# Optimization experiments

Measured on AMD Instinct MI355X. Metric: run time of the kernel, lower is better.

Reference implementation:

```python
import jax, jax.numpy as jnp
import numpy as np

INPUT_SIZE = 2048
HIDDEN_SIZE = 2048
BATCH = 4096


def setup_inputs() -> dict:
    key = jax.random.key(0)
    ks = jax.random.split(key, 24)
    s_in = 1.0 / np.sqrt(INPUT_SIZE)
    s_h = 1.0 / np.sqrt(HIDDEN_SIZE)
    inp = {
        "x": jax.random.normal(ks[0], (BATCH, INPUT_SIZE), jnp.float32),
        "h_prev": jax.random.normal(ks[1], (BATCH, HIDDEN_SIZE), jnp.float32),
        "c_prev": jax.random.normal(ks[2], (BATCH, HIDDEN_SIZE), jnp.float32),
        "n_prev": jnp.ones((BATCH, HIDDEN_SIZE), jnp.float32),
        "m_prev": jnp.zeros((BATCH, HIDDEN_SIZE), jnp.float32),
    }
    # 4 input projections (W*x) and 4 recurrent projections (R*h), each Linear w/ bias.
    names_x = ["Wzx", "Wix", "Wfx", "Wox"]
    names_h = ["Rzh", "Rih", "Rfh", "Roh"]
    for j, n in enumerate(names_x):
        inp[n + "_w"] = jax.random.uniform(ks[3 + 2 * j], (HIDDEN_SIZE, INPUT_SIZE), jnp.float32, -s_in, s_in)
        inp[n + "_b"] = jax.random.uniform(ks[4 + 2 * j], (HIDDEN_SIZE,), jnp.float32, -s_in, s_in)
    for j, n in enumerate(names_h):
        inp[n + "_w"] = jax.random.uniform(ks[11 + 2 * j], (HIDDEN_SIZE, HIDDEN_SIZE), jnp.float32, -s_h, s_h)
        inp[n + "_b"] = jax.random.uniform(ks[12 + 2 * j], (HIDDEN_SIZE,), jnp.float32, -s_h, s_h)
    return inp


def _lin(x, w, b):
    return x @ w.T + b


def reference(x, h_prev, c_prev, n_prev, m_prev,
              Wzx_w, Wzx_b, Wix_w, Wix_b, Wfx_w, Wfx_b, Wox_w, Wox_b,
              Rzh_w, Rzh_b, Rih_w, Rih_b, Rfh_w, Rfh_b, Roh_w, Roh_b):
    z = jnp.tanh(_lin(x, Wzx_w, Wzx_b) + _lin(h_prev, Rzh_w, Rzh_b))
    # log(i) and log(f) are the pre-activations (i = exp(pre_i), f = exp(pre_f))
    log_i = _lin(x, Wix_w, Wix_b) + _lin(h_prev, Rih_w, Rih_b)
    log_f = _lin(x, Wfx_w, Wfx_b) + _lin(h_prev, Rfh_w, Rfh_b)
    o = jax.nn.sigmoid(_lin(x, Wox_w, Wox_b) + _lin(h_prev, Roh_w, Roh_b))
    m = jnp.maximum(log_f + m_prev, log_i)  # stabilizer state
    i_hat = jnp.exp(log_i - m)
    f_hat = jnp.exp(log_f + m_prev - m)
    c = f_hat * c_prev + i_hat * z
    n = f_hat * n_prev + i_hat
    h = o * c / n
    return (h, c, n, m)
```

## Files before the change

### kernel.cpp

```cpp
#include <hip/hip_runtime.h>
#include <hip/hip_bf16.h>


#define BATCH 4096
#define NHID  2048
#define KDIM  4096
#define NTOT  8388608L
#define AW_OFS 16777216
#define BUFSZ 24576

typedef float  f32x4   __attribute__((ext_vector_type(4)));
typedef short  short8  __attribute__((ext_vector_type(8)));
typedef unsigned short ushort8 __attribute__((ext_vector_type(8)));

#define GL_LDS16(gp, lp)                                                      \
    __builtin_amdgcn_global_load_lds(                                         \
        (const __attribute__((address_space(1))) void*)(gp),                  \
        (__attribute__((address_space(3))) void*)(lp), 16, 0, 0)

__device__ __forceinline__ unsigned short f2bf(float f) {
    unsigned u = __float_as_uint(f);
    unsigned r = (u + 0x7fffu + ((u >> 16) & 1u)) >> 16;
    return (unsigned short)r;
}

__global__ void convA_kernel(const float* __restrict__ x,
                             const float* __restrict__ h,
                             unsigned short* __restrict__ A) {
    int gid = blockIdx.x * 256 + threadIdx.x;
    int row = gid >> 9;
    int col = (gid & 511) << 3;
    const float* src = (col < 2048) ? (x + (long)row * 2048 + col)
                                    : (h + (long)row * 2048 + (col - 2048));
    f32x4 v0 = __builtin_nontemporal_load((const f32x4*)src);
    f32x4 v1 = __builtin_nontemporal_load((const f32x4*)src + 1);
    ushort8 o;
    o[0] = f2bf(v0[0]); o[1] = f2bf(v0[1]); o[2] = f2bf(v0[2]); o[3] = f2bf(v0[3]);
    o[4] = f2bf(v1[0]); o[5] = f2bf(v1[1]); o[6] = f2bf(v1[2]); o[7] = f2bf(v1[3]);
    *(ushort8*)(A + ((long)row << 12) + col) = o;
}

__global__ void convW_kernel(const float* __restrict__ w0, const float* __restrict__ w1,
                             const float* __restrict__ w2, const float* __restrict__ w3,
                             const float* __restrict__ w4, const float* __restrict__ w5,
                             const float* __restrict__ w6, const float* __restrict__ w7,
                             unsigned short* __restrict__ Wb) {
    int z = blockIdx.y;
    const float* src;
    switch (z) {
        case 0: src = w0; break; case 1: src = w1; break;
        case 2: src = w2; break; case 3: src = w3; break;
        case 4: src = w4; break; case 5: src = w5; break;
        case 6: src = w6; break; default: src = w7; break;
    }
    int gid = blockIdx.x * 256 + threadIdx.x;
    int row = gid >> 8;
    int col = (gid & 255) << 3;
    const float* p = src + (long)row * 2048 + col;
    f32x4 v0 = __builtin_nontemporal_load((const f32x4*)p);
    f32x4 v1 = __builtin_nontemporal_load((const f32x4*)p + 1);
    ushort8 o;
    o[0] = f2bf(v0[0]); o[1] = f2bf(v0[1]); o[2] = f2bf(v0[2]); o[3] = f2bf(v0[3]);
    o[4] = f2bf(v1[0]); o[5] = f2bf(v1[1]); o[6] = f2bf(v1[2]); o[7] = f2bf(v1[3]);
    int g = z & 3, hf = z >> 2;
    *(ushort8*)(Wb + (long)g * NHID * KDIM + (long)row * KDIM + hf * 2048 + col) = o;
}

__global__ void bias_kernel(const float* __restrict__ b0, const float* __restrict__ b1,
                            const float* __restrict__ b2, const float* __restrict__ b3,
                            const float* __restrict__ r0, const float* __restrict__ r1,
                            const float* __restrict__ r2, const float* __restrict__ r3,
                            float* __restrict__ Bb) {
    int gid = blockIdx.x * 256 + threadIdx.x;
    int g = gid >> 11, j = gid & 2047;
    const float *wb, *rb;
    switch (g) {
        case 0: wb = b0; rb = r0; break; case 1: wb = b1; rb = r1; break;
        case 2: wb = b2; rb = r2; break; default: wb = b3; rb = r3; break;
    }
    Bb[gid] = wb[j] + rb[j];
}

__global__ __launch_bounds__(512, 4) void slstm_kernel(
    const __hip_bfloat16* __restrict__ A,
    const float* __restrict__ Bb,
    const float* __restrict__ c_prev,
    const float* __restrict__ n_prev,
    const float* __restrict__ m_prev,
    float* __restrict__ out)
{
    __shared__ uint4 smem4[(2 * BUFSZ) / 16];
    char* smem = (char*)smem4;

    const int tid  = threadIdx.x;
    const int lane = tid & 63;
    const int wv   = tid >> 6;
    const int gate = wv & 3;
    const int rh   = wv >> 2;
    const int lm   = lane & 15;
    const int quad = lane >> 4;

    const int row0 = blockIdx.x * 128;
    const int col0 = blockIdx.y * 64;

    const int cof   = ((quad ^ (lm & 3))) * 16;
    const int abase = (rh * 64 + lm) * 64 + cof;
    const int bbase = 8192 + (gate * 64 + lm) * 64 + cof;

    int gofs[3], lofs[3];
#pragma unroll
    for (int t = 0; t < 3; ++t) {
        int id = wv * 3 + t;
        if (id < 8) {
            int idx = id * 64 + lane;
            int r = idx >> 2, jj = idx & 3;
            int j = jj ^ (r & 3);
            gofs[t] = (row0 + r) * KDIM + j * 8;
            lofs[t] = idx * 16;
        } else {
            int idx = (id - 8) * 64 + lane;
            int gr = idx >> 2, jj = idx & 3;
            int g = gr >> 6, rr = gr & 63;
            int j = jj ^ (gr & 3);
            gofs[t] = AW_OFS + (g * NHID + col0 + rr) * KDIM + j * 8;
            lofs[t] = 8192 + idx * 16;
        }
    }

    f32x4 acc[4][4];
#pragma unroll
    for (int mt = 0; mt < 4; ++mt)
#pragma unroll
        for (int nt = 0; nt < 4; ++nt)
#pragma unroll
            for (int r = 0; r < 4; ++r) acc[mt][nt][r] = 0.0f;

#pragma unroll
    for (int t = 0; t < 3; ++t) {
        GL_LDS16(A + gofs[t], smem + lofs[t]);
        gofs[t] += 32;
    }

    for (int kt = 0; kt < 128; ++kt) {
        asm volatile("s_waitcnt vmcnt(0)" ::: "memory");
        __builtin_amdgcn_s_barrier();

        const char* cur = smem + (kt & 1) * BUFSZ;
        char*       wrt = smem + ((kt & 1) ^ 1) * BUFSZ;

        if (kt < 127) {
#pragma unroll
            for (int t = 0; t < 3; ++t) {
                GL_LDS16(A + gofs[t], wrt + lofs[t]);
                gofs[t] += 32;
            }
        }

        short8 af[4], bf[4];
#pragma unroll
        for (int mt = 0; mt < 4; ++mt)
            af[mt] = *(const short8*)(cur + abase + mt * 1024);
#pragma unroll
        for (int nt = 0; nt < 4; ++nt)
            bf[nt] = *(const short8*)(cur + bbase + nt * 1024);
#pragma unroll
        for (int mt = 0; mt < 4; ++mt)
#pragma unroll
            for (int nt = 0; nt < 4; ++nt)
                acc[mt][nt] = __builtin_amdgcn_mfma_f32_16x16x32_bf16(
                    af[mt], bf[nt], acc[mt][nt], 0, 0, 0);
    }

    float* exch = (float*)smem;
#pragma unroll
    for (int mt = 0; mt < 4; ++mt) {
        __syncthreads();
#pragma unroll
        for (int nt = 0; nt < 4; ++nt)
#pragma unroll
            for (int r = 0; r < 4; ++r)
                exch[((rh * 4 + gate) * 16 + quad * 4 + r) * 65 + nt * 16 + lm] =
                    acc[mt][nt][r];
        __syncthreads();
#pragma unroll
        for (int q = 0; q < 4; ++q) {
            int e   = q * 512 + tid;
            int erh = e >> 10, row = (e >> 6) & 15, col = e & 63;
            int R = row0 + erh * 64 + mt * 16 + row;
            int C = col0 + col;
            long idx = (long)R * NHID + C;
            float zp = exch[((erh * 4 + 0) * 16 + row) * 65 + col] + Bb[C];
            float ip = exch[((erh * 4 + 1) * 16 + row) * 65 + col] + Bb[2048 + C];
            float fp = exch[((erh * 4 + 2) * 16 + row) * 65 + col] + Bb[4096 + C];
            float op = exch[((erh * 4 + 3) * 16 + row) * 65 + col] + Bb[6144 + C];
            float cp = __builtin_nontemporal_load(c_prev + idx);
            float np = __builtin_nontemporal_load(n_prev + idx);
            float mp = __builtin_nontemporal_load(m_prev + idx);
            float z  = tanhf(zp);
            float o  = 1.0f / (1.0f + __expf(-op));
            float mm = fmaxf(fp + mp, ip);
            float ih = __expf(ip - mm);
            float fh = __expf(fp + mp - mm);
            float cc = fh * cp + ih * z;
            float nn = fh * np + ih;
            float hh = o * cc / nn;
            __builtin_nontemporal_store(hh, out + idx);
            __builtin_nontemporal_store(cc, out + NTOT + idx);
            __builtin_nontemporal_store(nn, out + 2 * NTOT + idx);
            __builtin_nontemporal_store(mm, out + 3 * NTOT + idx);
        }
    }
}

extern "C" void kernel_launch(void* const* d_in, const int* in_sizes, int n_in,
                              void* d_out, int out_size, void* d_ws, size_t ws_size,
                              hipStream_t stream) {
    const float* x      = (const float*)d_in[0];
    const float* h_prev = (const float*)d_in[1];
    const float* c_prev = (const float*)d_in[2];
    const float* n_prev = (const float*)d_in[3];
    const float* m_prev = (const float*)d_in[4];
    unsigned short* A  = (unsigned short*)d_ws;
    unsigned short* Wb = (unsigned short*)((char*)d_ws + 33554432);
    float*          Bb = (float*)((char*)d_ws + 100663296);

    convA_kernel<<<8192, 256, 0, stream>>>(x, h_prev, A);
    convW_kernel<<<dim3(2048, 8), 256, 0, stream>>>(
        (const float*)d_in[5], (const float*)d_in[7], (const float*)d_in[9],
        (const float*)d_in[11], (const float*)d_in[13], (const float*)d_in[15],
        (const float*)d_in[17], (const float*)d_in[19], Wb);
    bias_kernel<<<32, 256, 0, stream>>>(
        (const float*)d_in[6], (const float*)d_in[8], (const float*)d_in[10],
        (const float*)d_in[12], (const float*)d_in[14], (const float*)d_in[16],
        (const float*)d_in[18], (const float*)d_in[20], Bb);

    slstm_kernel<<<dim3(32, 32), 512, 0, stream>>>(
        (const __hip_bfloat16*)A, Bb, c_prev, n_prev, m_prev, (float*)d_out);
}
```

Baseline: 603.4 us.

## Repack A and W into k-chunk-major layout for contiguous LDS loads

The conversion kernels now write bf16 operands in a k-chunk-major packed layout, transposing through a small shared-memory tile, so that each 8-element k chunk for 64 consecutive rows is contiguous. The GEMM kernel's global-to-LDS loads then read fully contiguous 1 KB segments per wave instead of 16-byte pieces strided by a row, and the LDS fragment addressing drops the XOR swizzle. This aims to improve global load coalescing in the main GEMM loop. The cost is an extra LDS round trip and barrier in the conversion kernels, and LDS reads without a swizzle may hit bank conflicts.

Result: faster. 587.6 us (-2.6%).

```diff
diff --git a/kernel.cpp b/kernel.cpp
--- a/kernel.cpp
+++ b/kernel.cpp
@@ -26,26 +26,35 @@
 
 __global__ void convA_kernel(const float* __restrict__ x,
                              const float* __restrict__ h,
-                             unsigned short* __restrict__ A) {
-    int gid = blockIdx.x * 256 + threadIdx.x;
-    int row = gid >> 9;
-    int col = (gid & 511) << 3;
-    const float* src = (col < 2048) ? (x + (long)row * 2048 + col)
-                                    : (h + (long)row * 2048 + (col - 2048));
+                             unsigned short* __restrict__ Ap) {
+    __shared__ unsigned short tile[8][32][8];
+    const int t  = threadIdx.x;
+    const int r  = t >> 3, c8 = t & 7;
+    const int row = blockIdx.x * 32 + r;
+    const int k0  = blockIdx.y * 64;
+    const float* src = (blockIdx.y < 32)
+        ? (x + (long)row * 2048 + k0 + c8 * 8)
+        : (h + (long)row * 2048 + (k0 - 2048) + c8 * 8);
     f32x4 v0 = __builtin_nontemporal_load((const f32x4*)src);
     f32x4 v1 = __builtin_nontemporal_load((const f32x4*)src + 1);
     ushort8 o;
     o[0] = f2bf(v0[0]); o[1] = f2bf(v0[1]); o[2] = f2bf(v0[2]); o[3] = f2bf(v0[3]);
     o[4] = f2bf(v1[0]); o[5] = f2bf(v1[1]); o[6] = f2bf(v1[2]); o[7] = f2bf(v1[3]);
-    *(ushort8*)(A + ((long)row << 12) + col) = o;
+    *(ushort8*)&tile[c8][(r ^ (c8 << 2)) & 31][0] = o;
+    __syncthreads();
+    const int kcl = t >> 5, rr = t & 31;
+    ushort8 w = *(ushort8*)&tile[kcl][(rr ^ (kcl << 2)) & 31][0];
+    long dst = ((long)(blockIdx.y * 8 + kcl) * 4096 + blockIdx.x * 32 + rr) * 8;
+    __builtin_nontemporal_store(w, (ushort8*)(Ap + dst));
 }
 
 __global__ void convW_kernel(const float* __restrict__ w0, const float* __restrict__ w1,
                              const float* __restrict__ w2, const float* __restrict__ w3,
                              const float* __restrict__ w4, const float* __restrict__ w5,
                              const float* __restrict__ w6, const float* __restrict__ w7,
-                             unsigned short* __restrict__ Wb) {
-    int z = blockIdx.y;
+                             unsigned short* __restrict__ Wp) {
+    __shared__ unsigned short tile[8][32][8];
+    const int z = blockIdx.z;
     const float* src;
     switch (z) {
         case 0: src = w0; break; case 1: src = w1; break;
@@ -53,17 +62,24 @@
         case 4: src = w4; break; case 5: src = w5; break;
         case 6: src = w6; break; default: src = w7; break;
     }
-    int gid = blockIdx.x * 256 + threadIdx.x;
-    int row = gid >> 8;
-    int col = (gid & 255) << 3;
-    const float* p = src + (long)row * 2048 + col;
+    const int g = z & 3, hf = z >> 2;
+    const int t = threadIdx.x;
+    const int r = t >> 3, c8 = t & 7;
+    const int j  = blockIdx.x * 32 + r;
+    const int k2 = blockIdx.y * 64 + c8 * 8;
+    const float* p = src + (long)j * 2048 + k2;
     f32x4 v0 = __builtin_nontemporal_load((const f32x4*)p);
     f32x4 v1 = __builtin_nontemporal_load((const f32x4*)p + 1);
     ushort8 o;
     o[0] = f2bf(v0[0]); o[1] = f2bf(v0[1]); o[2] = f2bf(v0[2]); o[3] = f2bf(v0[3]);
     o[4] = f2bf(v1[0]); o[5] = f2bf(v1[1]); o[6] = f2bf(v1[2]); o[7] = f2bf(v1[3]);
-    int g = z & 3, hf = z >> 2;
-    *(ushort8*)(Wb + (long)g * NHID * KDIM + (long)row * KDIM + hf * 2048 + col) = o;
+    *(ushort8*)&tile[c8][(r ^ (c8 << 2)) & 31][0] = o;
+    __syncthreads();
+    const int kcl = t >> 5, rr = t & 31;
+    ushort8 w = *(ushort8*)&tile[kcl][(rr ^ (kcl << 2)) & 31][0];
+    const int kcg = hf * 256 + blockIdx.y * 8 + kcl;
+    long dst = ((long)kcg * 8192 + g * 2048 + blockIdx.x * 32 + rr) * 8;
+    __builtin_nontemporal_store(w, (ushort8*)(Wp + dst));
 }
 
 __global__ void bias_kernel(const float* __restrict__ b0, const float* __restrict__ b1,
@@ -82,7 +98,7 @@
 }
 
 __global__ __launch_bounds__(512, 4) void slstm_kernel(
-    const __hip_bfloat16* __restrict__ A,
+    const unsigned short* __restrict__ Ap,
     const float* __restrict__ Bb,
     const float* __restrict__ c_prev,
     const float* __restrict__ n_prev,
@@ -103,27 +119,24 @@
     const int row0 = blockIdx.x * 128;
     const int col0 = blockIdx.y * 64;
 
-    const int cof   = ((quad ^ (lm & 3))) * 16;
-    const int abase = (rh * 64 + lm) * 64 + cof;
-    const int bbase = 8192 + (gate * 64 + lm) * 64 + cof;
-
-    int gofs[3], lofs[3];
+    const int abase = quad * 2048 + (rh * 64 + lm) * 16;
+    const int bbase = 8192 + quad * 4096 + (gate * 64 + lm) * 16;
+
+    int gofs[3], strd[3], lofs[3];
 #pragma unroll
     for (int t = 0; t < 3; ++t) {
         int id = wv * 3 + t;
         if (id < 8) {
-            int idx = id * 64 + lane;
-            int r = idx >> 2, jj = idx & 3;
-            int j = jj ^ (r & 3);
-            gofs[t] = (row0 + r) * KDIM + j * 8;
-            lofs[t] = idx * 16;
+            int kc = id >> 1, half = id & 1;
+            gofs[t] = (kc * 4096 + row0 + half * 64 + lane) * 8;
+            strd[t] = 4 * 4096 * 8;
+            lofs[t] = id * 1024 + lane * 16;
         } else {
-            int idx = (id - 8) * 64 + lane;
-            int gr = idx >> 2, jj = idx & 3;
-            int g = gr >> 6, rr = gr & 63;
-            int j = jj ^ (gr & 3);
-            gofs[t] = AW_OFS + (g * NHID + col0 + rr) * KDIM + j * 8;
-            lofs[t] = 8192 + idx * 16;
+            int idb = id - 8;
+            int kc = idb >> 2, g = idb & 3;
+            gofs[t] = AW_OFS + (kc * 8192 + g * 2048 + col0 + lane) * 8;
+            strd[t] = 4 * 8192 * 8;
+            lofs[t] = 8192 + idb * 1024 + lane * 16;
         }
     }
 
@@ -137,8 +150,8 @@
 
 #pragma unroll
     for (int t = 0; t < 3; ++t) {
-        GL_LDS16(A + gofs[t], smem + lofs[t]);
-        gofs[t] += 32;
+        GL_LDS16(Ap + gofs[t], smem + lofs[t]);
+        gofs[t] += strd[t];
     }
 
     for (int kt = 0; kt < 128; ++kt) {
@@ -151,18 +164,18 @@
         if (kt < 127) {
 #pragma unroll
             for (int t = 0; t < 3; ++t) {
-                GL_LDS16(A + gofs[t], wrt + lofs[t]);
-                gofs[t] += 32;
+                GL_LDS16(Ap + gofs[t], wrt + lofs[t]);
+                gofs[t] += strd[t];
             }
         }
 
         short8 af[4], bf[4];
 #pragma unroll
         for (int mt = 0; mt < 4; ++mt)
-            af[mt] = *(const short8*)(cur + abase + mt * 1024);
+            af[mt] = *(const short8*)(cur + abase + mt * 256);
 #pragma unroll
         for (int nt = 0; nt < 4; ++nt)
-            bf[nt] = *(const short8*)(cur + bbase + nt * 1024);
+            bf[nt] = *(const short8*)(cur + bbase + nt * 256);
 #pragma unroll
         for (int mt = 0; mt < 4; ++mt)
 #pragma unroll
@@ -220,20 +233,20 @@
     const float* c_prev = (const float*)d_in[2];
     const float* n_prev = (const float*)d_in[3];
     const float* m_prev = (const float*)d_in[4];
-    unsigned short* A  = (unsigned short*)d_ws;
-    unsigned short* Wb = (unsigned short*)((char*)d_ws + 33554432);
+    unsigned short* Ap = (unsigned short*)d_ws;
+    unsigned short* Wp = (unsigned short*)((char*)d_ws + 33554432);
     float*          Bb = (float*)((char*)d_ws + 100663296);
 
-    convA_kernel<<<8192, 256, 0, stream>>>(x, h_prev, A);
-    convW_kernel<<<dim3(2048, 8), 256, 0, stream>>>(
+    convA_kernel<<<dim3(128, 64), 256, 0, stream>>>(x, h_prev, Ap);
+    convW_kernel<<<dim3(64, 32, 8), 256, 0, stream>>>(
         (const float*)d_in[5], (const float*)d_in[7], (const float*)d_in[9],
         (const float*)d_in[11], (const float*)d_in[13], (const float*)d_in[15],
-        (const float*)d_in[17], (const float*)d_in[19], Wb);
+        (const float*)d_in[17], (const float*)d_in[19], Wp);
     bias_kernel<<<32, 256, 0, stream>>>(
         (const float*)d_in[6], (const float*)d_in[8], (const float*)d_in[10],
         (const float*)d_in[12], (const float*)d_in[14], (const float*)d_in[16],
         (const float*)d_in[18], (const float*)d_in[20], Bb);
 
     slstm_kernel<<<dim3(32, 32), 512, 0, stream>>>(
-        (const __hip_bfloat16*)A, Bb, c_prev, n_prev, m_prev, (float*)d_out);
-}
+        Ap, Bb, c_prev, n_prev, m_prev, (float*)d_out);
+}
```
